# Kernel optimization log

Hardware: AMD Instinct MI355X
Metric: run time of the kernel (lower is better)

Reference implementation:

```python
import jax, jax.numpy as jnp
import numpy as np

N_NODES = 20000
N_EDGES = 50000
NF = 64
NG = 5
N_CONV = 2


def setup_inputs() -> dict:
    key = jax.random.key(0)
    ks = jax.random.split(key, 20)
    s = 0.1
    return {
        "h": jax.random.normal(ks[0], (N_NODES, 64), jnp.float32),
        "edge_index": jax.random.randint(ks[1], (2, N_EDGES), 0, N_NODES, jnp.int64),
        "edge_weight": jax.random.uniform(ks[2], (N_EDGES,), jnp.float32),
        "edge_attr": jax.random.normal(ks[3], (N_EDGES, NG), jnp.float32),
        # lin0: Linear(64 -> nf); stored as [in, out]
        "lin0_w": jax.random.normal(ks[4], (64, NF), jnp.float32) * s,
        "lin0_b": jnp.zeros((NF,), jnp.float32),
        # short: Linear(num_gaussians -> nf)
        "short_w": jax.random.normal(ks[5], (NG, NF), jnp.float32) * s,
        "short_b": jnp.zeros((NF,), jnp.float32),
        # edge network nn: Linear(nf -> nf//4) -> ReLU -> Linear(nf//4 -> nf*nf)
        "nn1_w": jax.random.normal(ks[6], (NF, NF // 4), jnp.float32) * s,
        "nn1_b": jnp.zeros((NF // 4,), jnp.float32),
        "nn2_w": jax.random.normal(ks[7], (NF // 4, NF * NF), jnp.float32) * s,
        "nn2_b": jnp.zeros((NF * NF,), jnp.float32),
        # NNConv root weight (Linear(nf, nf, bias=False)) + conv bias
        "root_w": jax.random.normal(ks[8], (NF, NF), jnp.float32) * s,
        "conv_bias": jnp.zeros((NF,), jnp.float32),
        # GRU(nf, nf): torch packs gates as [r; z; n] along dim 0 of [3*nf, nf]
        "gru_w_ih": jax.random.normal(ks[9], (NF, 3 * NF), jnp.float32) * s,
        "gru_w_hh": jax.random.normal(ks[10], (NF, 3 * NF), jnp.float32) * s,
        "gru_b_ih": jnp.zeros((3 * NF,), jnp.float32),
        "gru_b_hh": jnp.zeros((3 * NF,), jnp.float32),
    }


def _gru_cell(x, h, w_ih, w_hh, b_ih, b_hh):
    gi = x @ w_ih + b_ih            # [N, 3*nf]
    gh = h @ w_hh + b_hh
    r = jax.nn.sigmoid(gi[:, :NF] + gh[:, :NF])
    z = jax.nn.sigmoid(gi[:, NF:2 * NF] + gh[:, NF:2 * NF])
    n = jnp.tanh(gi[:, 2 * NF:] + r * gh[:, 2 * NF:])
    return (1.0 - z) * n + z * h


def reference(h, edge_index, edge_weight, edge_attr,
              lin0_w, lin0_b, short_w, short_b,
              nn1_w, nn1_b, nn2_w, nn2_b,
              root_w, conv_bias,
              gru_w_ih, gru_w_hh, gru_b_ih, gru_b_hh):
    n_nodes = h.shape[0]
    src, dst = edge_index[0], edge_index[1]

    out = jax.nn.relu(h @ lin0_w + lin0_b)                       # [N, nf]
    ea = jax.nn.relu(edge_attr @ short_w + short_b)              # [E, nf]

    # edge-conditioned weights (fixed per forward since edge_attr is fixed)
    w_e = (jax.nn.relu(ea @ nn1_w + nn1_b) @ nn2_w + nn2_b)      # [E, nf*nf]
    w_e = w_e.reshape(-1, NF, NF)                                # [E, nf, nf]

    # scatter-mean denominator (clamped to 1 like PyG)
    cnt = jax.ops.segment_sum(jnp.ones_like(dst, jnp.float32), dst,
                              num_segments=n_nodes)
    cnt = jnp.maximum(cnt, 1.0)[:, None]                          # [N, 1]

    hidden = out                                                  # GRU state [N, nf]
    for _ in range(N_CONV):
        x_j = out[src]                                            # gather [E, nf]
        msg = jnp.einsum('ef,efg->eg', x_j, w_e)                  # per-edge matmul
        agg = jax.ops.segment_sum(msg, dst, num_segments=n_nodes) / cnt
        conv = agg + out @ root_w + conv_bias                     # root + bias
        m = jax.nn.relu(conv)
        hidden = _gru_cell(m, hidden, gru_w_ih, gru_w_hh, gru_b_ih, gru_b_hh)
        out = hidden
    return out
```

## Files before the change

kernel.cpp:

```cpp
#include <hip/hip_runtime.h>

#define N_NODES 20000
#define N_EDGES 50000
#define NPB 16
#define KCAP 16
#define NTILE (N_NODES / NPB)

#define ZB 79
#define PB 416
#define LB 1250
#define ETB 3125
#define VB0 (ZB + PB + LB + ETB)
#define HB 196

typedef __attribute__((ext_vector_type(8))) short short8;
typedef __attribute__((ext_vector_type(4))) float f32x4;
typedef unsigned int u32;
typedef unsigned short u16;

#define SswzB(i, o) (((i) * 2304 + (o)) ^ (((i) & 7) << 4))
#define MofsB(i, o) ((20480 + (i) * 256 + (o)) ^ (((i) & 7) << 4))

struct Pars {
    const float* h; const int* ei; const float* eattr;
    const float *lin0w, *lin0b, *shw, *shb, *w1, *b1, *w2, *b2;
    const float *rootw, *convb, *wih, *whh, *bih, *bhh;
    float *X0, *X1, *out;
    u16 *t_arr, *Bp1, *Bp2;
    int* cur; u32* edata;
};

__device__ inline u16 f2bf(float x) {
    u32 u = __float_as_uint(x);
    return (u16)((u + 0x7FFFu + ((u >> 16) & 1u)) >> 16);
}

__device__ inline void acc_edge(float* acc, const u16* t, float x) {
    uint4 a = *(const uint4*)t, b = *(const uint4*)(t + 8);
    u32 tw[8] = {a.x, a.y, a.z, a.w, b.x, b.y, b.z, b.w};
#pragma unroll
    for (int q = 0; q < 8; ++q) {
        acc[2 * q]     += __uint_as_float(tw[q] << 16) * x;
        acc[2 * q + 1] += __uint_as_float(tw[q] & 0xFFFF0000u) * x;
    }
}

__global__ __launch_bounds__(256) void k_stageA(Pars p) {
    __shared__ float sh[16][64];
    int tid = threadIdx.x;
    int vb = blockIdx.x;
    if (vb < ZB) {
        int n = vb * 256 + tid;
        if (n < N_NODES) p.cur[n] = 0;
        return;
    }
    vb -= ZB;
    if (vb < PB) {
        int idx = vb * 256 + tid;
        if (idx < 73728) {
            int j = idx & 7, l = (idx >> 3) & 63, rest = idx >> 9;
            int kb = rest % 36, nt = rest / 36;
            int row = kb * 32 + (l >> 4) * 8 + j;
            int col = nt * 16 + (l & 15);
            float v;
            if (row < 1024) v = p.w2[row * 64 + col];
            else if (row < 1088) v = p.b2[(row - 1024) * 64 + col];
            else v = p.rootw[(row - 1088) * 64 + col];
            p.Bp1[idx] = f2bf(v);
        } else {
            int o = idx - 73728;
            int j = o & 7, l = (o >> 3) & 63, rest = o >> 9;
            int kb = rest & 3, nt = rest >> 2;
            int k2 = kb * 32 + (l >> 4) * 8 + j;
            int c = nt * 16 + (l & 15);
            float v;
            if (k2 < 64) {
                v = (c < 192) ? p.wih[k2 * 192 + c] : 0.f;
            } else {
                int f = k2 - 64;
                v = (c < 128) ? p.whh[f * 192 + c] : ((c < 192) ? 0.f : p.whh[f * 192 + c - 64]);
            }
            p.Bp2[o] = f2bf(v);
        }
        return;
    }
    vb -= PB;
    int g = tid & 63, q = tid >> 6;
    if (vb < LB) {
        int n0 = vb * 16;
        for (int i = tid; i < 16 * 64; i += 256) sh[i >> 6][i & 63] = p.h[n0 * 64 + i];
        __syncthreads();
        float acc[4] = {p.lin0b[g], p.lin0b[g], p.lin0b[g], p.lin0b[g]};
        for (int f = 0; f < 64; f++) {
            float wv = p.lin0w[f * 64 + g];
#pragma unroll
            for (int j = 0; j < 4; j++) acc[j] += sh[q * 4 + j][f] * wv;
        }
#pragma unroll
        for (int j = 0; j < 4; j++) {
            float a = acc[j];
            p.X0[(n0 + q * 4 + j) * 64 + g] = a > 0.f ? a : 0.f;
        }
        return;
    }
    vb -= LB;
    {
        int e0 = vb * 16;
#pragma unroll
        for (int j = 0; j < 4; j++) {
            int r = q * 4 + j;
            int e = e0 + r;
            float a0 = p.eattr[e * 5 + 0], a1 = p.eattr[e * 5 + 1], a2 = p.eattr[e * 5 + 2],
                  a3 = p.eattr[e * 5 + 3], a4 = p.eattr[e * 5 + 4];
            float v = p.shb[g] + a0 * p.shw[g] + a1 * p.shw[64 + g] + a2 * p.shw[128 + g]
                    + a3 * p.shw[192 + g] + a4 * p.shw[256 + g];
            sh[r][g] = v > 0.f ? v : 0.f;
        }
        __syncthreads();
        {
            int r = q * 4 + (g >> 4), o = g & 15;
            float acc = p.b1[o];
            for (int c = 0; c < 64; c++) acc += sh[r][c] * p.w1[c * 16 + o];
            float t = acc > 0.f ? acc : 0.f;
            p.t_arr[(size_t)(e0 + r) * 16 + o] = f2bf(t);
        }
    }
}

__global__ __launch_bounds__(256) void k_stageB(Pars p) {
    int e = blockIdx.x * 256 + threadIdx.x;
    if (e < N_EDGES) {
        int dn = p.ei[N_EDGES + e];
        int q = atomicAdd(&p.cur[dn], 1);
        if (q < KCAP) p.edata[dn * KCAP + q] = ((u32)e << 15) | (u32)p.ei[e];
    }
}

__global__ __launch_bounds__(256, 4) void k_convK(Pars p, const float* __restrict__ Xprev,
                                                  float* __restrict__ Xout) {
    __shared__ __align__(16) char smem[36864];
    float* G = (float*)smem;
    char* Sb = smem;
    int tid = threadIdx.x, g = tid & 63, wq = tid >> 6;
    int m16 = g & 15, hi4 = g >> 4;
    int n0 = blockIdx.x * NPB;

    int cvv[4];
    float xr4[4], ic4[4];
#pragma unroll
    for (int jj = 0; jj < 4; ++jj) {
        int n = n0 + wq * 4 + jj;
        int c = __builtin_amdgcn_readfirstlane(p.cur[n]);
        cvv[jj] = c < KCAP ? c : KCAP;
        ic4[jj] = 1.0f / (c > 0 ? (float)c : 1.0f);
        xr4[jj] = Xprev[n * 64 + g];
    }

    short8 a2x[2];
#pragma unroll
    for (int kb = 0; kb < 2; ++kb) {
        const float* xp = Xprev + (size_t)(n0 + m16) * 64 + kb * 32 + hi4 * 8;
        float4 xa = *(const float4*)xp;
        float4 xb = *(const float4*)(xp + 4);
        short8 av;
        av[0] = f2bf(xa.x); av[1] = f2bf(xa.y); av[2] = f2bf(xa.z); av[3] = f2bf(xa.w);
        av[4] = f2bf(xb.x); av[5] = f2bf(xb.y); av[6] = f2bf(xb.z); av[7] = f2bf(xb.w);
        a2x[kb] = av;
    }

    for (int jj = 0; jj < 4; ++jj) {
        int i = wq * 4 + jj;
        float acc[16];
#pragma unroll
        for (int k = 0; k < 16; ++k) acc[k] = 0.f;
        float sx = 0.f;
        int base = (n0 + i) * KCAP;
        int cv = cvv[jj];
        for (int pp = 0; pp < cv; pp += 4) {
            int m = cv - pp;
            uint4 ed = *(const uint4*)(p.edata + base + pp);
            u32 k0 = ed.x;
            u32 k1 = m > 1 ? ed.y : ed.x;
            u32 k2 = m > 2 ? ed.z : ed.x;
            u32 k3 = m > 3 ? ed.w : ed.x;
            float x0 = Xprev[(k0 & 0x7FFFu) * 64 + g];
            float x1 = m > 1 ? Xprev[(k1 & 0x7FFFu) * 64 + g] : 0.f;
            float x2 = m > 2 ? Xprev[(k2 & 0x7FFFu) * 64 + g] : 0.f;
            float x3 = m > 3 ? Xprev[(k3 & 0x7FFFu) * 64 + g] : 0.f;
            acc_edge(acc, p.t_arr + (size_t)(k0 >> 15) * 16, x0);
            acc_edge(acc, p.t_arr + (size_t)(k1 >> 15) * 16, x1);
            acc_edge(acc, p.t_arr + (size_t)(k2 >> 15) * 16, x2);
            acc_edge(acc, p.t_arr + (size_t)(k3 >> 15) * 16, x3);
            sx += x0 + x1 + x2 + x3;
        }
        float ic = ic4[jj];
#pragma unroll
        for (int k = 0; k < 16; ++k)
            *(u16*)(Sb + SswzB(i, k * 128 + g * 2)) = f2bf(acc[k] * ic);
        *(u16*)(Sb + SswzB(i, 2048 + g * 2)) = f2bf(sx * ic);
        *(u16*)(Sb + SswzB(i, 2176 + g * 2)) = f2bf(xr4[jj]);
    }
    __syncthreads();

    f32x4 d = {0.f, 0.f, 0.f, 0.f};
#pragma unroll
    for (int kb = 0; kb < 36; ++kb) {
        short8 a = *(const short8*)(Sb + SswzB(m16, kb * 64 + hi4 * 16));
        short8 b = *(const short8*)((const char*)p.Bp1 + ((size_t)(wq * 36 + kb) * 64 + g) * 16);
        d = __builtin_amdgcn_mfma_f32_16x16x32_bf16(a, b, d, 0, 0, 0);
    }
    __syncthreads();

    {
        float cb = p.convb[wq * 16 + m16];
#pragma unroll
        for (int r = 0; r < 4; ++r) {
            float m = d[r] + cb;
            m = m > 0.f ? m : 0.f;
            *(u16*)(smem + MofsB(hi4 * 4 + r, (wq * 16 + m16) * 2)) = f2bf(m);
        }
    }
    __syncthreads();

    short8 a2[4];
#pragma unroll
    for (int kb = 0; kb < 2; ++kb)
        a2[kb] = *(const short8*)(smem + MofsB(m16, kb * 64 + hi4 * 16));
    a2[2] = a2x[0];
    a2[3] = a2x[1];
    f32x4 e4[4];
#pragma unroll
    for (int q = 0; q < 4; ++q) { e4[q].x = 0.f; e4[q].y = 0.f; e4[q].z = 0.f; e4[q].w = 0.f; }
#pragma unroll
    for (int q = 0; q < 4; ++q)
#pragma unroll
        for (int kb = 0; kb < 4; ++kb) {
            short8 b = *(const short8*)((const char*)p.Bp2 + ((size_t)((wq * 4 + q) * 4 + kb) * 64 + g) * 16);
            e4[q] = __builtin_amdgcn_mfma_f32_16x16x32_bf16(a2[kb], b, e4[q], 0, 0, 0);
        }
#pragma unroll
    for (int q = 0; q < 4; ++q)
#pragma unroll
        for (int r = 0; r < 4; ++r)
            G[(hi4 * 4 + r) * 260 + wq * 64 + q * 16 + m16] = e4[q][r];
    __syncthreads();

    float b_r = p.bih[g] + p.bhh[g];
    float b_z = p.bih[64 + g] + p.bhh[64 + g];
    float b_gi = p.bih[128 + g];
    float b_gh = p.bhh[128 + g];
#pragma unroll
    for (int jj = 0; jj < 4; ++jj) {
        int i = wq * 4 + jj;
        int n = n0 + i;
        float rs = G[i * 260 + g] + b_r;
        float zs = G[i * 260 + 64 + g] + b_z;
        float gi = G[i * 260 + 128 + g] + b_gi;
        float gh = G[i * 260 + 192 + g] + b_gh;
        float r = 1.f / (1.f + __expf(-rs));
        float z = 1.f / (1.f + __expf(-zs));
        float aa = gi + r * gh;
        float ex = __expf(2.f * aa);
        float nt = 1.f - 2.f / (ex + 1.f);
        Xout[n * 64 + g] = (1.f - z) * nt + z * xr4[jj];
    }
}

extern "C" void kernel_launch(void* const* d_in, const int* in_sizes, int n_in,
                              void* d_out, int out_size, void* d_ws, size_t ws_size,
                              hipStream_t stream) {
    Pars p;
    p.h     = (const float*)d_in[0];
    p.ei    = (const int*)d_in[1];
    p.eattr = (const float*)d_in[3];
    p.lin0w = (const float*)d_in[4];
    p.lin0b = (const float*)d_in[5];
    p.shw   = (const float*)d_in[6];
    p.shb   = (const float*)d_in[7];
    p.w1    = (const float*)d_in[8];
    p.b1    = (const float*)d_in[9];
    p.w2    = (const float*)d_in[10];
    p.b2    = (const float*)d_in[11];
    p.rootw = (const float*)d_in[12];
    p.convb = (const float*)d_in[13];
    p.wih   = (const float*)d_in[14];
    p.whh   = (const float*)d_in[15];
    p.bih   = (const float*)d_in[16];
    p.bhh   = (const float*)d_in[17];

    char* ws = (char*)d_ws;
    p.X0    = (float*)ws; ws += (size_t)N_NODES * 64 * 4;
    p.X1    = (float*)ws; ws += (size_t)N_NODES * 64 * 4;
    p.t_arr = (u16*)ws;   ws += (size_t)N_EDGES * 16 * 2;
    p.Bp1   = (u16*)ws;   ws += (size_t)73728 * 2;
    p.Bp2   = (u16*)ws;   ws += (size_t)32768 * 2;
    p.cur   = (int*)ws;   ws += (size_t)N_NODES * 4;
    p.edata = (u32*)ws;   ws += (size_t)N_NODES * KCAP * 4;
    p.out   = (float*)d_out;

    k_stageA<<<VB0, 256, 0, stream>>>(p);
    k_stageB<<<HB, 256, 0, stream>>>(p);
    k_convK<<<NTILE, 256, 0, stream>>>(p, p.X0, p.X1);
    k_convK<<<NTILE, 256, 0, stream>>>(p, p.X1, p.out);
}
```

Before: 90.07 us.

## Store intermediate node features in bf16 and double per-block work in stage A

Intermediate node states X0/X1 are now stored as bf16 instead of fp32. This halves the bytes moved by the random neighbor gathers and by the node reads and writes in the conv kernels, and removes the fp32-to-bf16 conversion of the MFMA A operand. Stage A blocks now each process 32 nodes or edges instead of 16, with a bounds guard on the edge tail. The GRU residual now uses the bf16-rounded previous state, which adds some precision loss.

```diff
diff --git a/kernel.cpp b/kernel.cpp
--- a/kernel.cpp
+++ b/kernel.cpp
@@ -8,8 +8,8 @@
 
 #define ZB 79
 #define PB 416
-#define LB 1250
-#define ETB 3125
+#define LB 625
+#define ETB 1563
 #define VB0 (ZB + PB + LB + ETB)
 #define HB 196
 
@@ -25,7 +25,8 @@
     const float* h; const int* ei; const float* eattr;
     const float *lin0w, *lin0b, *shw, *shb, *w1, *b1, *w2, *b2;
     const float *rootw, *convb, *wih, *whh, *bih, *bhh;
-    float *X0, *X1, *out;
+    u16 *X0b, *X1b;
+    float* out;
     u16 *t_arr, *Bp1, *Bp2;
     int* cur; u32* edata;
 };
@@ -34,6 +35,7 @@
     u32 u = __float_as_uint(x);
     return (u16)((u + 0x7FFFu + ((u >> 16) & 1u)) >> 16);
 }
+__device__ inline float bf2f(u16 v) { return __uint_as_float((u32)v << 16); }
 
 __device__ inline void acc_edge(float* acc, const u16* t, float x) {
     uint4 a = *(const uint4*)t, b = *(const uint4*)(t + 8);
@@ -46,7 +48,7 @@
 }
 
 __global__ __launch_bounds__(256) void k_stageA(Pars p) {
-    __shared__ float sh[16][64];
+    __shared__ float sh[32][64];
     int tid = threadIdx.x;
     int vb = blockIdx.x;
     if (vb < ZB) {
@@ -87,42 +89,52 @@
     vb -= PB;
     int g = tid & 63, q = tid >> 6;
     if (vb < LB) {
-        int n0 = vb * 16;
-        for (int i = tid; i < 16 * 64; i += 256) sh[i >> 6][i & 63] = p.h[n0 * 64 + i];
+        int n0 = vb * 32;
+        for (int i = tid; i < 32 * 64; i += 256) sh[i >> 6][i & 63] = p.h[n0 * 64 + i];
         __syncthreads();
-        float acc[4] = {p.lin0b[g], p.lin0b[g], p.lin0b[g], p.lin0b[g]};
+        float bias = p.lin0b[g];
+        float acc[8];
+#pragma unroll
+        for (int j = 0; j < 8; j++) acc[j] = bias;
         for (int f = 0; f < 64; f++) {
             float wv = p.lin0w[f * 64 + g];
 #pragma unroll
-            for (int j = 0; j < 4; j++) acc[j] += sh[q * 4 + j][f] * wv;
-        }
-#pragma unroll
-        for (int j = 0; j < 4; j++) {
+            for (int j = 0; j < 8; j++) acc[j] += sh[q * 8 + j][f] * wv;
+        }
+#pragma unroll
+        for (int j = 0; j < 8; j++) {
             float a = acc[j];
-            p.X0[(n0 + q * 4 + j) * 64 + g] = a > 0.f ? a : 0.f;
+            p.X0b[(n0 + q * 8 + j) * 64 + g] = f2bf(a > 0.f ? a : 0.f);
         }
         return;
     }
     vb -= LB;
     {
-        int e0 = vb * 16;
-#pragma unroll
-        for (int j = 0; j < 4; j++) {
-            int r = q * 4 + j;
+        int e0 = vb * 32;
+#pragma unroll
+        for (int j = 0; j < 8; j++) {
+            int r = q * 8 + j;
             int e = e0 + r;
-            float a0 = p.eattr[e * 5 + 0], a1 = p.eattr[e * 5 + 1], a2 = p.eattr[e * 5 + 2],
-                  a3 = p.eattr[e * 5 + 3], a4 = p.eattr[e * 5 + 4];
-            float v = p.shb[g] + a0 * p.shw[g] + a1 * p.shw[64 + g] + a2 * p.shw[128 + g]
-                    + a3 * p.shw[192 + g] + a4 * p.shw[256 + g];
-            sh[r][g] = v > 0.f ? v : 0.f;
+            if (e < N_EDGES) {
+                float a0 = p.eattr[e * 5 + 0], a1 = p.eattr[e * 5 + 1], a2 = p.eattr[e * 5 + 2],
+                      a3 = p.eattr[e * 5 + 3], a4 = p.eattr[e * 5 + 4];
+                float v = p.shb[g] + a0 * p.shw[g] + a1 * p.shw[64 + g] + a2 * p.shw[128 + g]
+                        + a3 * p.shw[192 + g] + a4 * p.shw[256 + g];
+                sh[r][g] = v > 0.f ? v : 0.f;
+            }
         }
         __syncthreads();
-        {
-            int r = q * 4 + (g >> 4), o = g & 15;
-            float acc = p.b1[o];
-            for (int c = 0; c < 64; c++) acc += sh[r][c] * p.w1[c * 16 + o];
-            float t = acc > 0.f ? acc : 0.f;
-            p.t_arr[(size_t)(e0 + r) * 16 + o] = f2bf(t);
+#pragma unroll
+        for (int jj = 0; jj < 2; jj++) {
+            int r = q * 8 + (g >> 4) * 2 + jj;
+            int e = e0 + r;
+            int o = g & 15;
+            if (e < N_EDGES) {
+                float acc = p.b1[o];
+                for (int c = 0; c < 64; c++) acc += sh[r][c] * p.w1[c * 16 + o];
+                float t = acc > 0.f ? acc : 0.f;
+                p.t_arr[(size_t)e * 16 + o] = f2bf(t);
+            }
         }
     }
 }
@@ -136,8 +148,9 @@
     }
 }
 
-__global__ __launch_bounds__(256, 4) void k_convK(Pars p, const float* __restrict__ Xprev,
-                                                  float* __restrict__ Xout) {
+__global__ __launch_bounds__(256, 4) void k_convK(Pars p, const u16* __restrict__ Xprev,
+                                                  u16* __restrict__ XoutB,
+                                                  float* __restrict__ XoutF) {
     __shared__ __align__(16) char smem[36864];
     float* G = (float*)smem;
     char* Sb = smem;
@@ -146,27 +159,21 @@
     int n0 = blockIdx.x * NPB;
 
     int cvv[4];
-    float xr4[4], ic4[4];
+    u16 xrb[4];
+    float ic4[4];
 #pragma unroll
     for (int jj = 0; jj < 4; ++jj) {
         int n = n0 + wq * 4 + jj;
         int c = __builtin_amdgcn_readfirstlane(p.cur[n]);
         cvv[jj] = c < KCAP ? c : KCAP;
         ic4[jj] = 1.0f / (c > 0 ? (float)c : 1.0f);
-        xr4[jj] = Xprev[n * 64 + g];
+        xrb[jj] = Xprev[n * 64 + g];
     }
 
     short8 a2x[2];
 #pragma unroll
-    for (int kb = 0; kb < 2; ++kb) {
-        const float* xp = Xprev + (size_t)(n0 + m16) * 64 + kb * 32 + hi4 * 8;
-        float4 xa = *(const float4*)xp;
-        float4 xb = *(const float4*)(xp + 4);
-        short8 av;
-        av[0] = f2bf(xa.x); av[1] = f2bf(xa.y); av[2] = f2bf(xa.z); av[3] = f2bf(xa.w);
-        av[4] = f2bf(xb.x); av[5] = f2bf(xb.y); av[6] = f2bf(xb.z); av[7] = f2bf(xb.w);
-        a2x[kb] = av;
-    }
+    for (int kb = 0; kb < 2; ++kb)
+        a2x[kb] = *(const short8*)(Xprev + (size_t)(n0 + m16) * 64 + kb * 32 + hi4 * 8);
 
     for (int jj = 0; jj < 4; ++jj) {
         int i = wq * 4 + jj;
@@ -183,10 +190,10 @@
             u32 k1 = m > 1 ? ed.y : ed.x;
             u32 k2 = m > 2 ? ed.z : ed.x;
             u32 k3 = m > 3 ? ed.w : ed.x;
-            float x0 = Xprev[(k0 & 0x7FFFu) * 64 + g];
-            float x1 = m > 1 ? Xprev[(k1 & 0x7FFFu) * 64 + g] : 0.f;
-            float x2 = m > 2 ? Xprev[(k2 & 0x7FFFu) * 64 + g] : 0.f;
-            float x3 = m > 3 ? Xprev[(k3 & 0x7FFFu) * 64 + g] : 0.f;
+            float x0 = bf2f(Xprev[(k0 & 0x7FFFu) * 64 + g]);
+            float x1 = m > 1 ? bf2f(Xprev[(k1 & 0x7FFFu) * 64 + g]) : 0.f;
+            float x2 = m > 2 ? bf2f(Xprev[(k2 & 0x7FFFu) * 64 + g]) : 0.f;
+            float x3 = m > 3 ? bf2f(Xprev[(k3 & 0x7FFFu) * 64 + g]) : 0.f;
             acc_edge(acc, p.t_arr + (size_t)(k0 >> 15) * 16, x0);
             acc_edge(acc, p.t_arr + (size_t)(k1 >> 15) * 16, x1);
             acc_edge(acc, p.t_arr + (size_t)(k2 >> 15) * 16, x2);
@@ -198,7 +205,7 @@
         for (int k = 0; k < 16; ++k)
             *(u16*)(Sb + SswzB(i, k * 128 + g * 2)) = f2bf(acc[k] * ic);
         *(u16*)(Sb + SswzB(i, 2048 + g * 2)) = f2bf(sx * ic);
-        *(u16*)(Sb + SswzB(i, 2176 + g * 2)) = f2bf(xr4[jj]);
+        *(u16*)(Sb + SswzB(i, 2176 + g * 2)) = xrb[jj];
     }
     __syncthreads();
 
@@ -262,7 +269,9 @@
         float aa = gi + r * gh;
         float ex = __expf(2.f * aa);
         float nt = 1.f - 2.f / (ex + 1.f);
-        Xout[n * 64 + g] = (1.f - z) * nt + z * xr4[jj];
+        float res = (1.f - z) * nt + z * bf2f(xrb[jj]);
+        if (XoutF) XoutF[n * 64 + g] = res;
+        else       XoutB[n * 64 + g] = f2bf(res);
     }
 }
 
@@ -289,8 +298,8 @@
     p.bhh   = (const float*)d_in[17];
 
     char* ws = (char*)d_ws;
-    p.X0    = (float*)ws; ws += (size_t)N_NODES * 64 * 4;
-    p.X1    = (float*)ws; ws += (size_t)N_NODES * 64 * 4;
+    p.X0b   = (u16*)ws;   ws += (size_t)N_NODES * 64 * 2;
+    p.X1b   = (u16*)ws;   ws += (size_t)N_NODES * 64 * 2;
     p.t_arr = (u16*)ws;   ws += (size_t)N_EDGES * 16 * 2;
     p.Bp1   = (u16*)ws;   ws += (size_t)73728 * 2;
     p.Bp2   = (u16*)ws;   ws += (size_t)32768 * 2;
@@ -300,6 +309,6 @@
 
     k_stageA<<<VB0, 256, 0, stream>>>(p);
     k_stageB<<<HB, 256, 0, stream>>>(p);
-    k_convK<<<NTILE, 256, 0, stream>>>(p, p.X0, p.X1);
-    k_convK<<<NTILE, 256, 0, stream>>>(p, p.X1, p.out);
-}
+    k_convK<<<NTILE, 256, 0, stream>>>(p, p.X0b, p.X1b, nullptr);
+    k_convK<<<NTILE, 256, 0, stream>>>(p, p.X1b, nullptr, p.out);
+}
```

Measured after the change: 87.34 us, median of 2. -3.0%, faster.
